# Kernel tuning notes

Measured on AMD Instinct MI355X. Metric: run time of the kernel, lower is better.

The kernel has to match this reference:

```python
import jax, jax.numpy as jnp
import numpy as np

B, N, D = 256, 128, 512
NUM_TYPES, NUM_STATS = 6, 8
W_TYPE, W_STATS, W_CORR = 1.0, 1.0, 0.5
LN_EPS = 1e-5


def setup_inputs() -> dict:
    key = jax.random.key(0)
    ks = jax.random.split(key, 20)
    s = 1.0 / np.sqrt(D)
    inp = {
        "column_embeddings": jax.random.normal(ks[0], (B, N, D), jnp.float32),
        "masked_columns": jax.random.bernoulli(ks[1], 0.15, (B, N)),
        "type_targets": jax.random.randint(ks[2], (N,), 0, NUM_TYPES),
        "column_statistics": jax.random.normal(ks[3], (B, N, NUM_STATS), jnp.float32),
        "column_correlations": jnp.tanh(jax.random.normal(ks[4], (B, N, N), jnp.float32)),
        # type head: Linear(D,D) -> GELU -> LayerNorm -> Linear(D,NUM_TYPES)
        "t_W1": jax.random.normal(ks[5], (D, D), jnp.float32) * s,
        "t_b1": jnp.zeros((D,), jnp.float32),
        "t_g": jnp.ones((D,), jnp.float32),
        "t_beta": jnp.zeros((D,), jnp.float32),
        "t_W2": jax.random.normal(ks[6], (D, NUM_TYPES), jnp.float32) * s,
        "t_b2": jnp.zeros((NUM_TYPES,), jnp.float32),
        # stats head
        "s_W1": jax.random.normal(ks[7], (D, D), jnp.float32) * s,
        "s_b1": jnp.zeros((D,), jnp.float32),
        "s_g": jnp.ones((D,), jnp.float32),
        "s_beta": jnp.zeros((D,), jnp.float32),
        "s_W2": jax.random.normal(ks[8], (D, NUM_STATS), jnp.float32) * s,
        "s_b2": jnp.zeros((NUM_STATS,), jnp.float32),
        # bilinear correlation: x_i^T W x_j + b
        "c_W": jax.random.normal(ks[9], (D, D), jnp.float32) * s,
        "c_b": jnp.zeros((), jnp.float32),
    }
    return inp


def _mlp_head(x, W1, b1, g, beta, W2, b2):
    h = jax.nn.gelu(x @ W1 + b1, approximate=False)
    mu = h.mean(-1, keepdims=True)
    var = ((h - mu) ** 2).mean(-1, keepdims=True)
    h = (h - mu) * jax.lax.rsqrt(var + LN_EPS) * g + beta
    return h @ W2 + b2


def _forward(column_embeddings, masked_columns, type_targets,
             column_statistics, column_correlations,
             t_W1, t_b1, t_g, t_beta, t_W2, t_b2,
             s_W1, s_b1, s_g, s_beta, s_W2, s_b2,
             c_W, c_b):
    e = column_embeddings  # [B,N,D]
    type_logits = _mlp_head(e, t_W1, t_b1, t_g, t_beta, t_W2, t_b2)   # [B,N,T]
    stats_preds = _mlp_head(e, s_W1, s_b1, s_g, s_beta, s_W2, s_b2)   # [B,N,S]

    # batched bilinear correlation: tanh(e_i W e_j + b), diag forced to 1
    u = jnp.einsum('bnd,de->bne', e, c_W)            # [B,N,D]
    corr = jnp.tanh(jnp.einsum('bne,bme->bnm', u, e) + c_b)  # [B,N,N]
    eye = jnp.eye(e.shape[1], dtype=corr.dtype)
    corr = corr * (1.0 - eye) + eye

    m = masked_columns.astype(jnp.float32)           # [B,N]
    n_masked = jnp.maximum(m.sum(), 1.0)

    # type loss: masked-mean cross entropy; targets broadcast over batch
    logp = jax.nn.log_softmax(type_logits, axis=-1)
    tgt = jnp.broadcast_to(type_targets[None, :], m.shape)
    ce = -jnp.take_along_axis(logp, tgt[..., None], axis=-1)[..., 0]  # [B,N]
    type_loss = (ce * m).sum() / n_masked

    # stats loss: masked-mean MSE over [B,N,S]
    se = (stats_preds - column_statistics) ** 2
    stats_loss = (se * m[..., None]).sum() / (n_masked * se.shape[-1])

    # correlation loss: mask_expanded = m_i | m_j
    me = jnp.maximum(m[:, :, None], m[:, None, :])   # [B,N,N]
    n_me = jnp.maximum(me.sum(), 1.0)
    ce2 = (corr - column_correlations) ** 2
    correlation_loss = (ce2 * me).sum() / n_me

    total = W_TYPE * type_loss + W_STATS * stats_loss + W_CORR * correlation_loss
    return total


def reference(column_embeddings, masked_columns, type_targets,
              column_statistics, column_correlations,
              t_W1, t_b1, t_g, t_beta, t_W2, t_b2,
              s_W1, s_b1, s_g, s_beta, s_W2, s_b2,
              c_W, c_b):
    return _forward(column_embeddings, masked_columns, type_targets,
                    column_statistics, column_correlations,
                    t_W1, t_b1, t_g, t_beta, t_W2, t_b2,
                    s_W1, s_b1, s_g, s_beta, s_W2, s_b2,
                    c_W, c_b)
```

## Files before the change

kernel.cpp:

```cpp
#include <hip/hip_runtime.h>
#include <math.h>

#define Bx 256
#define Nx 128
#define Dx 512
#define Mx (Bx * Nx)
#define NTYPES 6
#define NSTATS 8
#define LN_EPS 1e-5f
#define CAP 8192

typedef __attribute__((ext_vector_type(8))) short frag8;
typedef __attribute__((ext_vector_type(4))) float f32x4;

__device__ __forceinline__ unsigned short f2bf(float f) {
    unsigned u = __float_as_uint(f);
    u += 0x7fff + ((u >> 16) & 1);
    return (unsigned short)(u >> 16);
}
__device__ __forceinline__ float bf2f(unsigned short s) {
    return __uint_as_float((unsigned)s << 16);
}

#define ASYNC16(g, l) __builtin_amdgcn_global_load_lds(                      \
    (const __attribute__((address_space(1))) void*)(g),                      \
    (__attribute__((address_space(3))) void*)(l), 16, 0, 0)

#define EB_OFF    0ULL
#define U_OFF     33554432ULL
#define HC_OFF    67108864ULL
#define WT_OFF    83886080ULL
#define WTC_OFF   84934656ULL
#define LIST_OFF  85458944ULL
#define CNTS_OFF  85590016ULL
#define PACC_OFF  85591040ULL
#define PCORR_OFF 85593088ULL
#define CNTP_OFF  85594112ULL

__global__ __launch_bounds__(256) void k_prep(
    const float* __restrict__ e, const float* __restrict__ W0,
    const float* __restrict__ W1, const float* __restrict__ W2,
    unsigned short* __restrict__ Eb, unsigned short* __restrict__ Tcmb,
    unsigned short* __restrict__ Tc, const int* __restrict__ m,
    int* __restrict__ list, int* __restrict__ cnts, int* cntp) {
    const int bid = blockIdx.x;
    const int t = threadIdx.x;
    if (bid < 256) {
        const int b = bid;
        const int r = b * Nx + t;
        int v = 0;
        if (t < 128) v = (m[r] != 0) ? 1 : 0;
        const unsigned long long bal = __ballot(v);
        const int wid = t >> 6, lane = t & 63;
        __shared__ int wcnt[2];
        __shared__ int base;
        if (lane == 0 && wid < 2) wcnt[wid] = __popcll(bal);
        __syncthreads();
        const int cnt = wcnt[0] + wcnt[1];
        if (t == 0) {
            base = atomicAdd(cntp, cnt);
            cnts[b] = cnt;
        }
        __syncthreads();
        if (t < 128 && v) {
            const int rank = __popcll(bal & ((1ULL << lane) - 1)) +
                             (wid ? wcnt[0] : 0);
            const int p = base + rank;
            if (p < CAP) list[p] = r;
        }
        return;
    }
    if (bid < 1024) {
        const int lin = (bid - 256) * 256 + t;
        const int mid = lin >> 16;
        const int i4  = (lin & 65535) * 4;
        const int n = i4 >> 9, k = i4 & 511;
        const float* W = (mid == 0) ? W0 : (mid == 1) ? W1 : W2;
        unsigned short* T = (mid == 2) ? Tc : (Tcmb + mid * 262144);
        unsigned short o[4];
#pragma unroll
        for (int j = 0; j < 4; ++j) o[j] = f2bf(W[(k + j) * Dx + n]);
        uint2 u;
        u.x = (unsigned)o[0] | ((unsigned)o[1] << 16);
        u.y = (unsigned)o[2] | ((unsigned)o[3] << 16);
        *(uint2*)(T + i4) = u;
        return;
    }
    const int r = (bid - 1024) * 4 + (t >> 6);
    const int lane = t & 63;
    const float4* src = (const float4*)(e + (size_t)r * Dx);
    const float4 a = src[lane * 2];
    const float4 b = src[lane * 2 + 1];
    unsigned short u[8] = {f2bf(a.x), f2bf(a.y), f2bf(a.z), f2bf(a.w),
                           f2bf(b.x), f2bf(b.y), f2bf(b.z), f2bf(b.w)};
    ((uint4*)(Eb + (size_t)r * Dx))[lane] = *(const uint4*)u;
}

__global__ __launch_bounds__(256) void k_gemms(
    const unsigned short* __restrict__ Eb,
    const unsigned short* __restrict__ Wtc,
    const unsigned short* __restrict__ Wtcmb,
    const float* __restrict__ bias0, const float* __restrict__ bias1,
    unsigned short* __restrict__ U, unsigned short* __restrict__ Hc,
    const int* __restrict__ list, const int* __restrict__ cntp) {
    __shared__ unsigned short As[128 * 32];
    __shared__ unsigned short Bs[128 * 32];
    const int bid = blockIdx.x;
    const int t = threadIdx.x;
    const unsigned short* Bt;
    unsigned short* C;
    int row0, col0, ldc, head, ra0, ra1;
    if (bid < 1024) {
        row0 = (bid >> 2) << 7;
        col0 = (bid & 3) << 7;
        Bt = Wtc; C = U; ldc = 512; head = 0;
        ra0 = row0 + (t >> 2);
        ra1 = ra0 + 64;
    } else {
        const int b2 = bid - 1024;
        row0 = (b2 >> 3) << 7;
        const int cnt = min(*cntp, CAP);
        if (row0 >= cnt) return;
        col0 = (b2 & 7) << 7;
        Bt = Wtcmb; C = Hc; ldc = 1024; head = 1;
        ra0 = list[min(row0 + (t >> 2), cnt - 1)];
        ra1 = list[min(row0 + 64 + (t >> 2), cnt - 1)];
    }
    const int w = t >> 6, l = t & 63;
    const int wr = (w >> 1) * 64, wcol = (w & 1) * 64;
    const int quad = l >> 4, mr = l & 15;

    const unsigned short* Ag0 = Eb + (size_t)ra0 * Dx + (t & 3) * 8;
    const unsigned short* Ag1 = Eb + (size_t)ra1 * Dx + (t & 3) * 8;
    const unsigned short* Bg0 = Bt + (size_t)(col0 + (t >> 2)) * Dx + (t & 3) * 8;
    const unsigned short* Bg1 = Bg0 + (size_t)64 * Dx;
    unsigned short* Al0 = As + t * 8;
    unsigned short* Al1 = As + (t + 256) * 8;
    unsigned short* Bl0 = Bs + t * 8;
    unsigned short* Bl1 = Bs + (t + 256) * 8;

    f32x4 acc[4][4] = {};
    for (int k0 = 0; k0 < Dx; k0 += 32) {
        __syncthreads();
        ASYNC16(Ag0 + k0, Al0);
        ASYNC16(Ag1 + k0, Al1);
        ASYNC16(Bg0 + k0, Bl0);
        ASYNC16(Bg1 + k0, Bl1);
        __syncthreads();
        frag8 a[4], b[4];
#pragma unroll
        for (int i = 0; i < 4; ++i)
            a[i] = *(const frag8*)&As[(wr + i * 16 + mr) * 32 + quad * 8];
#pragma unroll
        for (int j = 0; j < 4; ++j)
            b[j] = *(const frag8*)&Bs[(wcol + j * 16 + mr) * 32 + quad * 8];
#pragma unroll
        for (int i = 0; i < 4; ++i)
#pragma unroll
            for (int j = 0; j < 4; ++j)
                acc[i][j] = __builtin_amdgcn_mfma_f32_16x16x32_bf16(
                    a[i], b[j], acc[i][j], 0, 0, 0);
    }
#pragma unroll
    for (int i = 0; i < 4; ++i)
#pragma unroll
        for (int j = 0; j < 4; ++j)
#pragma unroll
            for (int r = 0; r < 4; ++r) {
                const int row = row0 + wr + i * 16 + quad * 4 + r;
                const int col = col0 + wcol + j * 16 + mr;
                float v = acc[i][j][r];
                if (head) {
                    v += (col < 512) ? bias0[col] : bias1[col - 512];
                    v = 0.5f * v * (1.0f + erff(v * 0.70710678118654752f));
                }
                C[(size_t)row * ldc + col] = f2bf(v);
            }
}

__global__ __launch_bounds__(256) void k_tail(
    const unsigned short* __restrict__ U,
    const unsigned short* __restrict__ Eb,
    const float* __restrict__ Ct, const int* __restrict__ m,
    const float* __restrict__ cbp, float* __restrict__ pcorr,
    const unsigned short* __restrict__ Hc,
    const float* __restrict__ tg, const float* __restrict__ tbeta,
    const float* __restrict__ tW2, const float* __restrict__ tb2,
    const float* __restrict__ sg, const float* __restrict__ sbeta,
    const float* __restrict__ sW2, const float* __restrict__ sb2,
    const int* __restrict__ list, const int* __restrict__ cntp,
    const int* __restrict__ tgt, const float* __restrict__ stats,
    float* __restrict__ pacc) {
    __shared__ unsigned short As[128 * 32];
    __shared__ unsigned short Bs[128 * 32];
    __shared__ float mloc[128];
    __shared__ float redf[4][2];
    const int t = threadIdx.x;
    const int w = t >> 6, l = t & 63;

    if (blockIdx.x < 256) {
        const int b = blockIdx.x;
        const int wr = (w >> 1) * 64, wcol = (w & 1) * 64;
        const int quad = l >> 4, mr = l & 15;
        if (t < 128) mloc[t] = (m[b * Nx + t] != 0) ? 1.0f : 0.0f;

        const unsigned short* Ub = U + (size_t)b * Nx * Dx;
        const unsigned short* E  = Eb + (size_t)b * Nx * Dx;
        const unsigned short* Ag0 = Ub + (size_t)(t >> 2) * Dx + (t & 3) * 8;
        const unsigned short* Ag1 = Ag0 + (size_t)64 * Dx;
        const unsigned short* Bg0 = E + (size_t)(t >> 2) * Dx + (t & 3) * 8;
        const unsigned short* Bg1 = Bg0 + (size_t)64 * Dx;
        unsigned short* Al0 = As + t * 8;
        unsigned short* Al1 = As + (t + 256) * 8;
        unsigned short* Bl0 = Bs + t * 8;
        unsigned short* Bl1 = Bs + (t + 256) * 8;

        f32x4 acc_r[4][4] = {};
        for (int k0 = 0; k0 < Dx; k0 += 32) {
            __syncthreads();
            ASYNC16(Ag0 + k0, Al0);
            ASYNC16(Ag1 + k0, Al1);
            ASYNC16(Bg0 + k0, Bl0);
            ASYNC16(Bg1 + k0, Bl1);
            __syncthreads();
            frag8 a[4], bfr[4];
#pragma unroll
            for (int i = 0; i < 4; ++i)
                a[i] = *(const frag8*)&As[(wr + i * 16 + mr) * 32 + quad * 8];
#pragma unroll
            for (int j = 0; j < 4; ++j)
                bfr[j] = *(const frag8*)&Bs[(wcol + j * 16 + mr) * 32 + quad * 8];
#pragma unroll
            for (int i = 0; i < 4; ++i)
#pragma unroll
                for (int j = 0; j < 4; ++j)
                    acc_r[i][j] = __builtin_amdgcn_mfma_f32_16x16x32_bf16(
                        a[i], bfr[j], acc_r[i][j], 0, 0, 0);
        }
        const float cb = cbp[0];
        float lsum = 0.0f;
#pragma unroll
        for (int i = 0; i < 4; ++i)
#pragma unroll
            for (int j = 0; j < 4; ++j)
#pragma unroll
                for (int r = 0; r < 4; ++r) {
                    const int row = wr + i * 16 + quad * 4 + r;
                    const int col = wcol + j * 16 + mr;
                    float c = (row == col) ? 1.0f : tanhf(acc_r[i][j][r] + cb);
                    const float me = fmaxf(mloc[row], mloc[col]);
                    const float d = c - Ct[((size_t)b * Nx + row) * Nx + col];
                    lsum += me * d * d;
                }
#pragma unroll
        for (int off = 32; off > 0; off >>= 1) lsum += __shfl_down(lsum, off);
        if (l == 0) redf[w][0] = lsum;
        __syncthreads();
        if (t == 0) pcorr[b] = redf[0][0] + redf[1][0] + redf[2][0] + redf[3][0];
        return;
    }

    const int blk = blockIdx.x - 256;
    const int cnt = min(*cntp, CAP);
    float ce_acc = 0.0f, sse_acc = 0.0f;
    for (int idx = blk * 4 + w; idx < cnt; idx += 256 * 4) {
        const int r = list[idx];
        const uint4 ut = ((const uint4*)(Hc + (size_t)idx * 1024))[l];
        const uint4 us = ((const uint4*)(Hc + (size_t)idx * 1024 + 512))[l];
        float a[8], b8[8];
        {
            const unsigned uu[4] = {ut.x, ut.y, ut.z, ut.w};
            const unsigned vv[4] = {us.x, us.y, us.z, us.w};
#pragma unroll
            for (int j = 0; j < 4; ++j) {
                a[2 * j]      = bf2f((unsigned short)(uu[j] & 0xffff));
                a[2 * j + 1]  = bf2f((unsigned short)(uu[j] >> 16));
                b8[2 * j]     = bf2f((unsigned short)(vv[j] & 0xffff));
                b8[2 * j + 1] = bf2f((unsigned short)(vv[j] >> 16));
            }
        }
        float st = 0, qt = 0, ss = 0, qs = 0;
#pragma unroll
        for (int j = 0; j < 8; ++j) {
            st += a[j]; qt += a[j] * a[j];
            ss += b8[j]; qs += b8[j] * b8[j];
        }
#pragma unroll
        for (int off = 32; off > 0; off >>= 1) {
            st += __shfl_xor(st, off); qt += __shfl_xor(qt, off);
            ss += __shfl_xor(ss, off); qs += __shfl_xor(qs, off);
        }
        const float mt = st * (1.0f / Dx);
        const float rt = rsqrtf(qt * (1.0f / Dx) - mt * mt + LN_EPS);
        const float ms = ss * (1.0f / Dx);
        const float rs = rsqrtf(qs * (1.0f / Dx) - ms * ms + LN_EPS);

        const int c0 = l * 8;
        float tp[6] = {}, sp[8] = {};
#pragma unroll
        for (int j = 0; j < 8; ++j) {
            const int c = c0 + j;
            const float nt = (a[j] - mt) * rt * tg[c] + tbeta[c];
#pragma unroll
            for (int k = 0; k < 6; ++k) tp[k] += nt * tW2[c * 6 + k];
            const float ns = (b8[j] - ms) * rs * sg[c] + sbeta[c];
#pragma unroll
            for (int k = 0; k < 8; ++k) sp[k] += ns * sW2[c * 8 + k];
        }
#pragma unroll
        for (int k = 0; k < 6; ++k)
#pragma unroll
            for (int off = 32; off > 0; off >>= 1) tp[k] += __shfl_down(tp[k], off);
#pragma unroll
        for (int k = 0; k < 8; ++k)
#pragma unroll
            for (int off = 32; off > 0; off >>= 1) sp[k] += __shfl_down(sp[k], off);

        if (l == 0) {
            float lg[6];
#pragma unroll
            for (int k = 0; k < 6; ++k) lg[k] = tp[k] + tb2[k];
            float mx = lg[0];
#pragma unroll
            for (int k = 1; k < 6; ++k) mx = fmaxf(mx, lg[k]);
            float se = 0.0f;
#pragma unroll
            for (int k = 0; k < 6; ++k) se += expf(lg[k] - mx);
            ce_acc += -(lg[tgt[r & (Nx - 1)]] - mx - logf(se));
            float sse = 0.0f;
#pragma unroll
            for (int k = 0; k < 8; ++k) {
                const float d = sp[k] + sb2[k] - stats[(size_t)r * NSTATS + k];
                sse += d * d;
            }
            sse_acc += sse;
        }
    }
    if (l == 0) { redf[w][0] = ce_acc; redf[w][1] = sse_acc; }
    __syncthreads();
    if (t == 0) {
        pacc[2 * blk]     = redf[0][0] + redf[1][0] + redf[2][0] + redf[3][0];
        pacc[2 * blk + 1] = redf[0][1] + redf[1][1] + redf[2][1] + redf[3][1];
    }
}

__global__ __launch_bounds__(256) void k_final(
    const float* __restrict__ pacc, const float* __restrict__ pcorr,
    const int* __restrict__ cnts, const int* __restrict__ cntp,
    float* __restrict__ out) {
    const int t = threadIdx.x, w = t >> 6, lane = t & 63;
    float ce = pacc[2 * t], sse = pacc[2 * t + 1], co = pcorr[t];
    const int c = cnts[t];
    float me = (float)(Nx * Nx) - (float)((Nx - c) * (Nx - c));
#pragma unroll
    for (int off = 32; off > 0; off >>= 1) {
        ce += __shfl_down(ce, off);
        sse += __shfl_down(sse, off);
        co += __shfl_down(co, off);
        me += __shfl_down(me, off);
    }
    __shared__ float red[4][4];
    if (lane == 0) {
        red[w][0] = ce; red[w][1] = sse; red[w][2] = co; red[w][3] = me;
    }
    __syncthreads();
    if (t == 0) {
        const float CE = red[0][0] + red[1][0] + red[2][0] + red[3][0];
        const float SSE = red[0][1] + red[1][1] + red[2][1] + red[3][1];
        const float CO = red[0][2] + red[1][2] + red[2][2] + red[3][2];
        const float ME = red[0][3] + red[1][3] + red[2][3] + red[3][3];
        const float nm = fmaxf((float)*cntp, 1.0f);
        const float nme = fmaxf(ME, 1.0f);
        out[0] = CE / nm + SSE / (nm * (float)NSTATS) + 0.5f * CO / nme;
    }
}

extern "C" void kernel_launch(void* const* d_in, const int* in_sizes, int n_in,
                              void* d_out, int out_size, void* d_ws, size_t ws_size,
                              hipStream_t stream) {
    const float* e      = (const float*)d_in[0];
    const int*   mcols  = (const int*)d_in[1];
    const int*   ttgt   = (const int*)d_in[2];
    const float* stats  = (const float*)d_in[3];
    const float* corrT  = (const float*)d_in[4];
    const float* tW1    = (const float*)d_in[5];
    const float* tb1    = (const float*)d_in[6];
    const float* tg     = (const float*)d_in[7];
    const float* tbeta  = (const float*)d_in[8];
    const float* tW2    = (const float*)d_in[9];
    const float* tb2    = (const float*)d_in[10];
    const float* sW1    = (const float*)d_in[11];
    const float* sb1    = (const float*)d_in[12];
    const float* sg     = (const float*)d_in[13];
    const float* sbeta  = (const float*)d_in[14];
    const float* sW2    = (const float*)d_in[15];
    const float* sb2    = (const float*)d_in[16];
    const float* cW     = (const float*)d_in[17];
    const float* cb     = (const float*)d_in[18];
    float* out = (float*)d_out;

    char* ws = (char*)d_ws;
    unsigned short* Eb    = (unsigned short*)(ws + EB_OFF);
    unsigned short* U     = (unsigned short*)(ws + U_OFF);
    unsigned short* Hc    = (unsigned short*)(ws + HC_OFF);
    unsigned short* Wtcmb = (unsigned short*)(ws + WT_OFF);
    unsigned short* Wtc   = (unsigned short*)(ws + WTC_OFF);
    int*   list  = (int*)(ws + LIST_OFF);
    int*   cnts  = (int*)(ws + CNTS_OFF);
    float* pacc  = (float*)(ws + PACC_OFF);
    float* pcorr = (float*)(ws + PCORR_OFF);
    int*   cntp  = (int*)(ws + CNTP_OFF);

    hipMemsetAsync(cntp, 0, sizeof(int), stream);
    k_prep<<<9216, 256, 0, stream>>>(e, tW1, sW1, cW, Eb, Wtcmb, Wtc, mcols,
                                     list, cnts, cntp);
    k_gemms<<<1536, 256, 0, stream>>>(Eb, Wtc, Wtcmb, tb1, sb1, U, Hc, list, cntp);
    k_tail<<<512, 256, 0, stream>>>(U, Eb, corrT, mcols, cb, pcorr,
                                    Hc, tg, tbeta, tW2, tb2, sg, sbeta, sW2, sb2,
                                    list, cntp, ttgt, stats, pacc);
    k_final<<<1, 256, 0, stream>>>(pacc, pcorr, cnts, cntp, out);
}
```

Before: 248.2 us.

## Double-buffer LDS tiles and XOR-swizzle k-chunks in MFMA GEMM loops

Both GEMM loops (the projection/head GEMMs and the per-batch bilinear GEMM) now use two LDS buffers, so the async global-to-LDS load of the next k-slice is issued before the MFMAs on the current slice. This is meant to hide load latency behind compute. The k-chunk within each 32-element row is also XOR-swizzled on the global source side and again on the fragment read side, to reduce LDS bank conflicts. The cost is double the LDS per block, which may lower occupancy. Correctness depends on the swizzle being applied consistently on the load and read sides.

```diff
diff --git a/kernel.cpp b/kernel.cpp
--- a/kernel.cpp
+++ b/kernel.cpp
@@ -25,6 +25,37 @@
 #define ASYNC16(g, l) __builtin_amdgcn_global_load_lds(                      \
     (const __attribute__((address_space(1))) void*)(g),                      \
     (__attribute__((address_space(3))) void*)(l), 16, 0, 0)
+
+__device__ __forceinline__ void stage4(const unsigned short* Ag0,
+                                       const unsigned short* Ag1,
+                                       const unsigned short* Bg0,
+                                       const unsigned short* Bg1, int k0,
+                                       unsigned short* Asl, unsigned short* Bsl,
+                                       int t) {
+    ASYNC16(Ag0 + k0, Asl + t * 8);
+    ASYNC16(Ag1 + k0, Asl + (t + 256) * 8);
+    ASYNC16(Bg0 + k0, Bsl + t * 8);
+    ASYNC16(Bg1 + k0, Bsl + (t + 256) * 8);
+}
+
+__device__ __forceinline__ void mfma_step(const unsigned short* Asl,
+                                          const unsigned short* Bsl,
+                                          int wr, int wcol, int mr, int aswz,
+                                          f32x4 acc[4][4]) {
+    frag8 a[4], b[4];
+#pragma unroll
+    for (int i = 0; i < 4; ++i)
+        a[i] = *(const frag8*)&Asl[(wr + i * 16 + mr) * 32 + aswz];
+#pragma unroll
+    for (int j = 0; j < 4; ++j)
+        b[j] = *(const frag8*)&Bsl[(wcol + j * 16 + mr) * 32 + aswz];
+#pragma unroll
+    for (int i = 0; i < 4; ++i)
+#pragma unroll
+        for (int j = 0; j < 4; ++j)
+            acc[i][j] = __builtin_amdgcn_mfma_f32_16x16x32_bf16(
+                a[i], b[j], acc[i][j], 0, 0, 0);
+}
 
 #define EB_OFF    0ULL
 #define U_OFF     33554432ULL
@@ -103,8 +134,8 @@
     const float* __restrict__ bias0, const float* __restrict__ bias1,
     unsigned short* __restrict__ U, unsigned short* __restrict__ Hc,
     const int* __restrict__ list, const int* __restrict__ cntp) {
-    __shared__ unsigned short As[128 * 32];
-    __shared__ unsigned short Bs[128 * 32];
+    __shared__ unsigned short As[2][4096];
+    __shared__ unsigned short Bs[2][4096];
     const int bid = blockIdx.x;
     const int t = threadIdx.x;
     const unsigned short* Bt;
@@ -129,37 +160,24 @@
     const int w = t >> 6, l = t & 63;
     const int wr = (w >> 1) * 64, wcol = (w & 1) * 64;
     const int quad = l >> 4, mr = l & 15;
-
-    const unsigned short* Ag0 = Eb + (size_t)ra0 * Dx + (t & 3) * 8;
-    const unsigned short* Ag1 = Eb + (size_t)ra1 * Dx + (t & 3) * 8;
-    const unsigned short* Bg0 = Bt + (size_t)(col0 + (t >> 2)) * Dx + (t & 3) * 8;
+    const int gswz = (((t & 3) ^ ((t >> 2) & 3)) - (t & 3)) * 8;
+    const int aswz = (quad ^ (mr & 3)) * 8;
+
+    const unsigned short* Ag0 = Eb + (size_t)ra0 * Dx + (t & 3) * 8 + gswz;
+    const unsigned short* Ag1 = Eb + (size_t)ra1 * Dx + (t & 3) * 8 + gswz;
+    const unsigned short* Bg0 = Bt + (size_t)(col0 + (t >> 2)) * Dx + (t & 3) * 8 + gswz;
     const unsigned short* Bg1 = Bg0 + (size_t)64 * Dx;
-    unsigned short* Al0 = As + t * 8;
-    unsigned short* Al1 = As + (t + 256) * 8;
-    unsigned short* Bl0 = Bs + t * 8;
-    unsigned short* Bl1 = Bs + (t + 256) * 8;
 
     f32x4 acc[4][4] = {};
-    for (int k0 = 0; k0 < Dx; k0 += 32) {
+    stage4(Ag0, Ag1, Bg0, Bg1, 0, As[0], Bs[0], t);
+    for (int k0 = 0; k0 < Dx; k0 += 64) {
         __syncthreads();
-        ASYNC16(Ag0 + k0, Al0);
-        ASYNC16(Ag1 + k0, Al1);
-        ASYNC16(Bg0 + k0, Bl0);
-        ASYNC16(Bg1 + k0, Bl1);
+        stage4(Ag0, Ag1, Bg0, Bg1, k0 + 32, As[1], Bs[1], t);
+        mfma_step(As[0], Bs[0], wr, wcol, mr, aswz, acc);
         __syncthreads();
-        frag8 a[4], b[4];
-#pragma unroll
-        for (int i = 0; i < 4; ++i)
-            a[i] = *(const frag8*)&As[(wr + i * 16 + mr) * 32 + quad * 8];
-#pragma unroll
-        for (int j = 0; j < 4; ++j)
-            b[j] = *(const frag8*)&Bs[(wcol + j * 16 + mr) * 32 + quad * 8];
-#pragma unroll
-        for (int i = 0; i < 4; ++i)
-#pragma unroll
-            for (int j = 0; j < 4; ++j)
-                acc[i][j] = __builtin_amdgcn_mfma_f32_16x16x32_bf16(
-                    a[i], b[j], acc[i][j], 0, 0, 0);
+        if (k0 + 64 < Dx)
+            stage4(Ag0, Ag1, Bg0, Bg1, k0 + 64, As[0], Bs[0], t);
+        mfma_step(As[1], Bs[1], wr, wcol, mr, aswz, acc);
     }
 #pragma unroll
     for (int i = 0; i < 4; ++i)
@@ -191,8 +209,8 @@
     const int* __restrict__ list, const int* __restrict__ cntp,
     const int* __restrict__ tgt, const float* __restrict__ stats,
     float* __restrict__ pacc) {
-    __shared__ unsigned short As[128 * 32];
-    __shared__ unsigned short Bs[128 * 32];
+    __shared__ unsigned short As[2][4096];
+    __shared__ unsigned short Bs[2][4096];
     __shared__ float mloc[128];
     __shared__ float redf[4][2];
     const int t = threadIdx.x;
@@ -204,38 +222,25 @@
         const int quad = l >> 4, mr = l & 15;
         if (t < 128) mloc[t] = (m[b * Nx + t] != 0) ? 1.0f : 0.0f;
 
+        const int gswz = (((t & 3) ^ ((t >> 2) & 3)) - (t & 3)) * 8;
+        const int aswz = (quad ^ (mr & 3)) * 8;
         const unsigned short* Ub = U + (size_t)b * Nx * Dx;
         const unsigned short* E  = Eb + (size_t)b * Nx * Dx;
-        const unsigned short* Ag0 = Ub + (size_t)(t >> 2) * Dx + (t & 3) * 8;
+        const unsigned short* Ag0 = Ub + (size_t)(t >> 2) * Dx + (t & 3) * 8 + gswz;
         const unsigned short* Ag1 = Ag0 + (size_t)64 * Dx;
-        const unsigned short* Bg0 = E + (size_t)(t >> 2) * Dx + (t & 3) * 8;
+        const unsigned short* Bg0 = E + (size_t)(t >> 2) * Dx + (t & 3) * 8 + gswz;
         const unsigned short* Bg1 = Bg0 + (size_t)64 * Dx;
-        unsigned short* Al0 = As + t * 8;
-        unsigned short* Al1 = As + (t + 256) * 8;
-        unsigned short* Bl0 = Bs + t * 8;
-        unsigned short* Bl1 = Bs + (t + 256) * 8;
 
         f32x4 acc_r[4][4] = {};
-        for (int k0 = 0; k0 < Dx; k0 += 32) {
+        stage4(Ag0, Ag1, Bg0, Bg1, 0, As[0], Bs[0], t);
+        for (int k0 = 0; k0 < Dx; k0 += 64) {
             __syncthreads();
-            ASYNC16(Ag0 + k0, Al0);
-            ASYNC16(Ag1 + k0, Al1);
-            ASYNC16(Bg0 + k0, Bl0);
-            ASYNC16(Bg1 + k0, Bl1);
+            stage4(Ag0, Ag1, Bg0, Bg1, k0 + 32, As[1], Bs[1], t);
+            mfma_step(As[0], Bs[0], wr, wcol, mr, aswz, acc_r);
             __syncthreads();
-            frag8 a[4], bfr[4];
-#pragma unroll
-            for (int i = 0; i < 4; ++i)
-                a[i] = *(const frag8*)&As[(wr + i * 16 + mr) * 32 + quad * 8];
-#pragma unroll
-            for (int j = 0; j < 4; ++j)
-                bfr[j] = *(const frag8*)&Bs[(wcol + j * 16 + mr) * 32 + quad * 8];
-#pragma unroll
-            for (int i = 0; i < 4; ++i)
-#pragma unroll
-                for (int j = 0; j < 4; ++j)
-                    acc_r[i][j] = __builtin_amdgcn_mfma_f32_16x16x32_bf16(
-                        a[i], bfr[j], acc_r[i][j], 0, 0, 0);
+            if (k0 + 64 < Dx)
+                stage4(Ag0, Ag1, Bg0, Bg1, k0 + 64, As[0], Bs[0], t);
+            mfma_step(As[1], Bs[1], wr, wcol, mr, aswz, acc_r);
         }
         const float cb = cbp[0];
         float lsum = 0.0f;
```

New measurement: 254.8 us. 2.7% more time.
